# Kernel optimization log

Hardware: AMD Instinct MI355X
Metric: run time of the kernel (lower is better)

## Reference

```python
import jax, jax.numpy as jnp
import numpy as np

NUM_TYPES = 60
TOK_DIM = 128
DIM_TOK = TOK_DIM + 1          # +1 sentinel bucket
SMALL = 2
C = NUM_TYPES + DIM_TOK + SMALL  # 191 channels
STEPS = 10
BLOCKS = 5
NTYPES_E = 3
N = 4000
E = 12000
G = 32
LN_EPS = 1e-5


def setup_inputs() -> dict:
    key = jax.random.key(0)
    ks = jax.random.split(key, 12)
    p = lambda k, shape: jax.random.normal(k, shape, dtype=jnp.float32) * 0.02
    return dict(
        x_small=jax.random.uniform(ks[0], (N, SMALL), dtype=jnp.float32),
        conv_w=p(ks[1], (BLOCKS, NTYPES_E, STEPS, C, C)),
        gru_wih=p(ks[2], (BLOCKS, NTYPES_E, 3 * C, C)),
        gru_whh=p(ks[3], (BLOCKS, NTYPES_E, 3 * C, C)),
        gru_bih=jnp.zeros((BLOCKS, NTYPES_E, 3 * C), jnp.float32),
        gru_bhh=jnp.zeros((BLOCKS, NTYPES_E, 3 * C), jnp.float32),
        ln_w=jnp.ones((BLOCKS, C), jnp.float32),
        ln_b=jnp.zeros((BLOCKS, C), jnp.float32),
        head_w1=p(ks[4], (C, C)),
        head_b1=jnp.zeros((C,), jnp.float32),
        head_w2=p(ks[5], (C, 2)),
        head_b2=jnp.zeros((2,), jnp.float32),
        x_type=jax.random.randint(ks[6], (N,), 0, NUM_TYPES),
        x_tok=jax.random.randint(ks[7], (N,), 0, DIM_TOK),
        edge_index=jax.random.randint(ks[8], (2, E), 0, N),
        edge_type=jax.random.randint(ks[9], (E,), 0, NTYPES_E),
        batch=jnp.sort(jax.random.randint(ks[10], (N,), 0, G)),
    )


def reference(x_small, conv_w, gru_wih, gru_whh, gru_bih, gru_bhh,
              ln_w, ln_b, head_w1, head_b1, head_w2, head_b2,
              x_type, x_tok, edge_index, edge_type, batch):
    n = x_type.shape[0]
    # build_features: one-hot type || one-hot hashed token || small floats
    h_type = jax.nn.one_hot(x_type, NUM_TYPES, dtype=jnp.float32)
    h_tok = jax.nn.one_hot(jnp.clip(x_tok, 0, DIM_TOK - 1), DIM_TOK, dtype=jnp.float32)
    h = jnp.concatenate([h_type, h_tok, x_small], axis=1)  # [N, C]
    src, dst = edge_index[0], edge_index[1]

    def gated_conv(h0, w_steps, wih, whh, bih, bhh, emask):
        # PyG GatedGraphConv: per step, m = x @ W_i; scatter-add m[src]->dst; x = GRUCell(agg, x)
        def step(x, wi):
            m = x @ wi  # [N, C]
            agg = jax.ops.segment_sum(m[src] * emask[:, None], dst, num_segments=n)
            gi = agg @ wih.T + bih  # [N, 3C] input gates (r,z,n order as in torch)
            gh = x @ whh.T + bhh
            ir, iz, ic = jnp.split(gi, 3, axis=-1)
            hr, hz, hc = jnp.split(gh, 3, axis=-1)
            r = jax.nn.sigmoid(ir + hr)
            z = jax.nn.sigmoid(iz + hz)
            c = jnp.tanh(ic + r * hc)
            return (1.0 - z) * c + z * x, None
        x, _ = jax.lax.scan(step, h0, w_steps)
        return x

    for b in range(BLOCKS):
        h_msg = jnp.zeros_like(h)
        for t in range(NTYPES_E):
            # edge-type masking as zero-weight scatter (same math as boolean slicing)
            emask = (edge_type == t).astype(h.dtype)
            h_msg = h_msg + gated_conv(h, conv_w[b, t], gru_wih[b, t], gru_whh[b, t],
                                       gru_bih[b, t], gru_bhh[b, t], emask)
        x = h + h_msg
        mu = jnp.mean(x, axis=-1, keepdims=True)
        var = jnp.mean((x - mu) ** 2, axis=-1, keepdims=True)
        h = jax.nn.relu((x - mu) * jax.lax.rsqrt(var + LN_EPS) * ln_w[b] + ln_b[b])
        # dropout is identity in eval mode

    # global_mean_pool
    counts = jax.ops.segment_sum(jnp.ones((n,), h.dtype), batch, num_segments=G)
    hg = jax.ops.segment_sum(h, batch, num_segments=G) / jnp.maximum(counts, 1.0)[:, None]
    z1 = jax.nn.relu(hg @ head_w1 + head_b1)
    return z1 @ head_w2 + head_b2  # [G, 2] logits
```

## Files before the change

### kernel.cpp

```cpp
#include <hip/hip_runtime.h>
#include <math.h>

#define N_NODES 4000
#define CC 191
#define CP 192
#define NT 3
#define NB 5
#define NS 10
#define EE 12000
#define GG 32
#define THREE_C 573
#define NC (N_NODES * CP)
#define NPAD 576

typedef __attribute__((ext_vector_type(8))) short short8;
typedef __attribute__((ext_vector_type(4))) float f32x4;

__device__ __forceinline__ unsigned short f2bf(float f) {
    unsigned u = __float_as_uint(f);
    unsigned r = (u + 0x7fffu + ((u >> 16) & 1u)) >> 16;
    return (unsigned short)r;
}
__device__ __forceinline__ float bf2f(unsigned short s) {
    return __uint_as_float(((unsigned)s) << 16);
}
__device__ __forceinline__ float dot4(float4 a, float4 b) {
    return a.x * b.x + a.y * b.y + a.z * b.z + a.w * b.w;
}
__device__ __forceinline__ void dma16(const void* g, void* l) {
    __builtin_amdgcn_global_load_lds(
        (const __attribute__((address_space(1))) unsigned int*)g,
        (__attribute__((address_space(3))) unsigned int*)l, 16, 0, 0);
}

__global__ void k_build_h(const float* __restrict__ xs, const int* __restrict__ xtype,
                          const int* __restrict__ xtok, float* __restrict__ h) {
    int idx = blockIdx.x * 256 + threadIdx.x;
    if (idx >= NC) return;
    int i = idx / CP, c = idx % CP;
    float v = 0.f;
    if (c < 60) {
        v = (xtype[i] == c) ? 1.f : 0.f;
    } else if (c < 189) {
        int tk = xtok[i];
        tk = tk < 0 ? 0 : (tk > 128 ? 128 : tk);
        v = (tk == c - 60) ? 1.f : 0.f;
    } else if (c < CC) {
        v = xs[i * 2 + (c - 189)];
    }
    h[idx] = v;
}

__global__ void k_pad_conv(const float* __restrict__ w, float* __restrict__ wp) {
    long idx = (long)blockIdx.x * 256 + threadIdx.x;
    if (idx >= 150L * 192 * 192) return;
    int b = (int)(idx / (192 * 192));
    int r = (int)((idx / 192) % 192);
    int c = (int)(idx % 192);
    wp[idx] = (r < CC && c < CC) ? w[(long)b * CC * CC + (long)r * CC + c] : 0.f;
}

__global__ void k_pad573(const float* __restrict__ w, float* __restrict__ wp, int batches) {
    long tot = (long)batches * THREE_C * CP;
    long idx = (long)blockIdx.x * 256 + threadIdx.x;
    if (idx >= tot) return;
    int b = (int)(idx / (THREE_C * CP));
    int r = (int)((idx / CP) % THREE_C);
    int c = (int)(idx % CP);
    wp[idx] = (c < CC) ? w[((long)b * THREE_C + r) * CC + c] : 0.f;
}

__global__ void k_edge_count(const int* __restrict__ ei, const int* __restrict__ et,
                             int* __restrict__ cnt) {
    int e = blockIdx.x * 256 + threadIdx.x;
    if (e >= EE) return;
    atomicAdd(&cnt[et[e] * N_NODES + ei[EE + e]], 1);
}

__global__ void k_scan(const int* __restrict__ cnt, int* __restrict__ off, int* __restrict__ fill) {
    const int TOT = NT * N_NODES;
    const int CH = (TOT + 255) / 256;
    __shared__ int ls[256];
    int tid = threadIdx.x;
    int base = tid * CH;
    int s = 0;
    for (int u = 0; u < CH; u++) {
        int idx = base + u;
        if (idx < TOT) s += cnt[idx];
    }
    ls[tid] = s;
    __syncthreads();
    for (int d = 1; d < 256; d <<= 1) {
        int v = 0;
        if (tid >= d) v = ls[tid - d];
        __syncthreads();
        if (tid >= d) ls[tid] += v;
        __syncthreads();
    }
    int run = (tid > 0) ? ls[tid - 1] : 0;
    for (int u = 0; u < CH; u++) {
        int idx = base + u;
        if (idx < TOT) {
            off[idx] = run;
            fill[idx] = run;
            run += cnt[idx];
        }
    }
    if (tid == 255) off[TOT] = run;
}

__global__ void k_edge_fill(const int* __restrict__ ei, const int* __restrict__ et,
                            int* __restrict__ fill, int* __restrict__ csrc) {
    int e = blockIdx.x * 256 + threadIdx.x;
    if (e >= EE) return;
    int pos = atomicAdd(&fill[et[e] * N_NODES + ei[EE + e]], 1);
    csrc[pos] = ei[e];
}

__global__ __launch_bounds__(256) void k_fmat(const float* __restrict__ wih_p,
                                              const float* __restrict__ conv_wp,
                                              float* __restrict__ F_t, int b) {
    int ts = blockIdx.z;
    int t = ts / NS;
    int j30 = blockIdx.x * 32;
    int k0 = blockIdx.y * 64;
    const float* A = wih_p + (long)(b * 3 + t) * THREE_C * CP;
    const float* B = conv_wp + ((long)b * 30 + ts) * 192 * 192;
    __shared__ float sA[32 * 52];
    __shared__ float sB[64 * 52];
    int tid = threadIdx.x;
    int tj = tid % 32;
    int tn = tid / 32;
    float acc0[4] = {0, 0, 0, 0}, acc1[4] = {0, 0, 0, 0};
    for (int kb = 0; kb < 4; kb++) {
        int q0 = kb * 48;
        for (int idx = tid; idx < 32 * 12; idx += 256) {
            int row = idx / 12, c4 = idx % 12;
            int j3 = j30 + row; j3 = j3 < THREE_C ? j3 : THREE_C - 1;
            *(float4*)(sA + row * 52 + c4 * 4) = *(const float4*)(A + (long)j3 * CP + q0 + c4 * 4);
        }
        for (int idx = tid; idx < 64 * 12; idx += 256) {
            int row = idx / 12, c4 = idx % 12;
            *(float4*)(sB + row * 52 + c4 * 4) = *(const float4*)(B + (long)(k0 + row) * CP + q0 + c4 * 4);
        }
        __syncthreads();
        #pragma unroll 3
        for (int q4 = 0; q4 < 12; q4++) {
            float4 bv0 = *(const float4*)(sB + tj * 52 + q4 * 4);
            float4 bv1 = *(const float4*)(sB + (tj + 32) * 52 + q4 * 4);
            #pragma unroll
            for (int u = 0; u < 4; u++) {
                float4 av = *(const float4*)(sA + (tn + 8 * u) * 52 + q4 * 4);
                acc0[u] += dot4(av, bv0);
                acc1[u] += dot4(av, bv1);
            }
        }
        __syncthreads();
    }
    #pragma unroll
    for (int u = 0; u < 4; u++) {
        int j3 = j30 + tn + 8 * u;
        if (j3 < THREE_C) {
            F_t[((long)ts * THREE_C + j3) * CP + k0 + tj] = acc0[u];
            F_t[((long)ts * THREE_C + j3) * CP + k0 + tj + 32] = acc1[u];
        }
    }
}

__global__ void k_convF(const float* __restrict__ F_t, unsigned short* __restrict__ FH,
                        unsigned short* __restrict__ FL) {
    long idx = (long)blockIdx.x * 256 + threadIdx.x;
    if (idx >= 30L * NPAD * CP) return;
    int k = (int)(idx % CP);
    int p = (int)((idx / CP) % NPAD);
    int ts = (int)(idx / ((long)NPAD * CP));
    int B0 = p / 96, pr = p % 96;
    int v = pr >> 4, u = pr & 15;
    int g = v % 3;
    int j = B0 * 32 + (v / 3) * 16 + u;
    float val = 0.f;
    if (j < CC) val = F_t[((long)ts * THREE_C + g * CC + j) * CP + k];
    unsigned short hi = f2bf(val);
    FH[idx] = hi;
    FL[idx] = f2bf(val - bf2f(hi));
}

__global__ void k_convW(const float* __restrict__ whh_p, unsigned short* __restrict__ WH,
                        unsigned short* __restrict__ WL, int b) {
    long idx = (long)blockIdx.x * 256 + threadIdx.x;
    if (idx >= 3L * NPAD * CP) return;
    int k = (int)(idx % CP);
    int p = (int)((idx / CP) % NPAD);
    int t = (int)(idx / ((long)NPAD * CP));
    int B0 = p / 96, pr = p % 96;
    int v = pr >> 4, u = pr & 15;
    int g = v % 3;
    int j = B0 * 32 + (v / 3) * 16 + u;
    float val = 0.f;
    if (j < CC) val = whh_p[((long)(b * 3 + t) * THREE_C + g * CC + j) * CP + k];
    unsigned short hi = f2bf(val);
    WH[idx] = hi;
    WL[idx] = f2bf(val - bf2f(hi));
}

__global__ void k_split3(const float* __restrict__ h, unsigned short* __restrict__ XH,
                         unsigned short* __restrict__ XL) {
    int idx = blockIdx.x * 256 + threadIdx.x;
    if (idx >= NC) return;
    float f = h[idx];
    unsigned short hi = f2bf(f);
    unsigned short lo = f2bf(f - bf2f(hi));
    #pragma unroll
    for (int t = 0; t < NT; t++) {
        XH[(long)t * NC + idx] = hi;
        XL[(long)t * NC + idx] = lo;
    }
}

__global__ void k_agg(const unsigned short* __restrict__ XH, const unsigned short* __restrict__ XL,
                      unsigned short* __restrict__ AH, unsigned short* __restrict__ AL,
                      const int* __restrict__ off, const int* __restrict__ csrc) {
    int node = blockIdx.x;
    int t = blockIdx.y;
    int k = threadIdx.x;
    const unsigned short* Xh = XH + (long)t * NC;
    const unsigned short* Xl = XL + (long)t * NC;
    int e0 = off[t * N_NODES + node];
    int e1 = off[t * N_NODES + node + 1];
    float s = 0.f;
    for (int e = e0; e < e1; e++) {
        long base = (long)csrc[e] * CP + k;
        s += bf2f(Xh[base]) + bf2f(Xl[base]);
    }
    unsigned short hi = f2bf(s);
    long o = ((long)t * N_NODES + node) * CP + k;
    AH[o] = hi;
    AL[o] = f2bf(s - bf2f(hi));
}

__global__ __launch_bounds__(256, 2) void k_step(
        const unsigned short* __restrict__ XcH, const unsigned short* __restrict__ XcL,
        const unsigned short* __restrict__ AgH, const unsigned short* __restrict__ AgL,
        const unsigned short* __restrict__ FH, const unsigned short* __restrict__ FL,
        const unsigned short* __restrict__ WH, const unsigned short* __restrict__ WL,
        const float* __restrict__ bih, const float* __restrict__ bhh,
        unsigned short* __restrict__ XnH, unsigned short* __restrict__ XnL,
        int b, int s) {
    const int t = blockIdx.z;
    const int ts = t * NS + s;
    const int M0 = blockIdx.x * 128;
    const int N0 = blockIdx.y * 96;

    __shared__ __align__(16) char smem[57344];

    const int tid = threadIdx.x;
    const int lane = tid & 63;
    const int wave = tid >> 6;
    const int wm = wave & 1;
    const int wn = wave >> 1;
    const int l15 = lane & 15;
    const int kb = lane >> 4;
    const int quad = lane >> 4;

    const unsigned short* gA[4];
    gA[0] = XcH + (size_t)t * NC;
    gA[1] = AgH + (size_t)t * NC;
    gA[2] = XcL + (size_t)t * NC;
    gA[3] = AgL + (size_t)t * NC;
    const unsigned short* gB[4];
    gB[0] = FH + (size_t)ts * NPAD * CP;
    gB[1] = WH + (size_t)t * NPAD * CP;
    gB[2] = FL + (size_t)ts * NPAD * CP;
    gB[3] = WL + (size_t)t * NPAD * CP;

    f32x4 accGI[4][3], accGH[4][3];
    #pragma unroll
    for (int mi = 0; mi < 4; mi++)
        #pragma unroll
        for (int nj = 0; nj < 3; nj++) {
            accGI[mi][nj] = (f32x4){0.f, 0.f, 0.f, 0.f};
            accGH[mi][nj] = (f32x4){0.f, 0.f, 0.f, 0.f};
        }

    const int ldso = (tid & 192) << 4;
    const int qsA = tid & 3;
    const int rA_lo = tid >> 2;

    for (int k = 0; k < 6; k++) {
        const int ko = k * 32;
        __syncthreads();
        #pragma unroll
        for (int i = 0; i < 8; i++) {
            int a = i >> 1;
            int r = (i & 1) * 64 + rA_lo;
            int q = qsA ^ ((r >> 1) & 3);
            int node = M0 + r; node = node < N_NODES ? node : N_NODES - 1;
            dma16(gA[a] + (size_t)node * CP + ko + q * 8, smem + i * 4096 + ldso);
        }
        #pragma unroll
        for (int i = 0; i < 6; i++) {
            int c = i * 256 + tid;
            int a = c / 384;
            int rem = c - a * 384;
            int r = rem >> 2, qs = rem & 3;
            int q = qs ^ ((r >> 1) & 3);
            dma16(gB[a] + (size_t)(N0 + r) * CP + ko + q * 8, smem + 32768 + i * 4096 + ldso);
        }
        __syncthreads();

        short8 xh[4], gh[4], xl[4], gl[4];
        #pragma unroll
        for (int mi = 0; mi < 4; mi++) {
            int r = wm * 64 + mi * 16 + l15;
            int sl = (r * 4 + (kb ^ ((r >> 1) & 3))) * 16;
            xh[mi] = *(const short8*)(smem + sl);
            gh[mi] = *(const short8*)(smem + 8192 + sl);
            xl[mi] = *(const short8*)(smem + 16384 + sl);
            gl[mi] = *(const short8*)(smem + 24576 + sl);
        }
        short8 fh[3], wh[3], fl[3], wl[3];
        #pragma unroll
        for (int nj = 0; nj < 3; nj++) {
            int r = wn * 48 + nj * 16 + l15;
            int sl = (r * 4 + (kb ^ ((r >> 1) & 3))) * 16;
            fh[nj] = *(const short8*)(smem + 32768 + sl);
            wh[nj] = *(const short8*)(smem + 38912 + sl);
            fl[nj] = *(const short8*)(smem + 45056 + sl);
            wl[nj] = *(const short8*)(smem + 51200 + sl);
        }
        #pragma unroll
        for (int mi = 0; mi < 4; mi++)
            #pragma unroll
            for (int nj = 0; nj < 3; nj++) {
                accGI[mi][nj] = __builtin_amdgcn_mfma_f32_16x16x32_bf16(
                    gh[mi], fh[nj], accGI[mi][nj], 0, 0, 0);
                accGI[mi][nj] = __builtin_amdgcn_mfma_f32_16x16x32_bf16(
                    gl[mi], fh[nj], accGI[mi][nj], 0, 0, 0);
                accGI[mi][nj] = __builtin_amdgcn_mfma_f32_16x16x32_bf16(
                    gh[mi], fl[nj], accGI[mi][nj], 0, 0, 0);
                accGH[mi][nj] = __builtin_amdgcn_mfma_f32_16x16x32_bf16(
                    xh[mi], wh[nj], accGH[mi][nj], 0, 0, 0);
                accGH[mi][nj] = __builtin_amdgcn_mfma_f32_16x16x32_bf16(
                    xl[mi], wh[nj], accGH[mi][nj], 0, 0, 0);
                accGH[mi][nj] = __builtin_amdgcn_mfma_f32_16x16x32_bf16(
                    xh[mi], wl[nj], accGH[mi][nj], 0, 0, 0);
            }
    }

    const int J = blockIdx.y * 32 + wn * 16 + l15;
    const bool jv = (J < CC);
    const int Je = jv ? J : 0;
    const int bo = (b * 3 + t) * THREE_C;
    const float bir = bih[bo + Je], biz = bih[bo + CC + Je], bic = bih[bo + 2 * CC + Je];
    const float bhr = bhh[bo + Je], bhz = bhh[bo + CC + Je], bhc = bhh[bo + 2 * CC + Je];
    #pragma unroll
    for (int mi = 0; mi < 4; mi++) {
        #pragma unroll
        for (int r = 0; r < 4; r++) {
            int node = M0 + wm * 64 + mi * 16 + quad * 4 + r;
            if (node < N_NODES && jv) {
                size_t xi = (size_t)(t * N_NODES + node) * CP + J;
                float xold = bf2f(XcH[xi]) + bf2f(XcL[xi]);
                float rr = 1.f / (1.f + expf(-(accGI[mi][0][r] + bir + accGH[mi][0][r] + bhr)));
                float zz = 1.f / (1.f + expf(-(accGI[mi][1][r] + biz + accGH[mi][1][r] + bhz)));
                float cg = tanhf(accGI[mi][2][r] + bic + rr * (accGH[mi][2][r] + bhc));
                float outv = (1.f - zz) * cg + zz * xold;
                unsigned short oh = f2bf(outv);
                XnH[xi] = oh;
                XnL[xi] = f2bf(outv - bf2f(oh));
            }
        }
    }
}

__global__ void k_ln(float* __restrict__ h, const unsigned short* __restrict__ XH,
                     const unsigned short* __restrict__ XL,
                     const float* __restrict__ lnw, const float* __restrict__ lnb, int b) {
    int i = blockIdx.x;
    int c = threadIdx.x;
    long base = (long)i * CP + c;
    float v = 0.f;
    if (c < CC) {
        v = h[base];
        #pragma unroll
        for (int t = 0; t < NT; t++)
            v += bf2f(XH[(long)t * NC + base]) + bf2f(XL[(long)t * NC + base]);
    }
    float sv = v;
    for (int o = 32; o > 0; o >>= 1) sv += __shfl_down(sv, o);
    __shared__ float ls[3];
    __shared__ float bc[2];
    if ((threadIdx.x & 63) == 0) ls[threadIdx.x >> 6] = sv;
    __syncthreads();
    if (threadIdx.x == 0) bc[0] = (ls[0] + ls[1] + ls[2]) / (float)CC;
    __syncthreads();
    float mu = bc[0];
    float d = (c < CC) ? (v - mu) : 0.f;
    float s2 = d * d;
    for (int o = 32; o > 0; o >>= 1) s2 += __shfl_down(s2, o);
    __syncthreads();
    if ((threadIdx.x & 63) == 0) ls[threadIdx.x >> 6] = s2;
    __syncthreads();
    if (threadIdx.x == 0) bc[1] = (ls[0] + ls[1] + ls[2]) / (float)CC;
    __syncthreads();
    float var = bc[1];
    float y = 0.f;
    if (c < CC) {
        y = d * rsqrtf(var + 1e-5f) * lnw[b * CC + c] + lnb[b * CC + c];
        y = y > 0.f ? y : 0.f;
    }
    h[base] = y;
}

__global__ void k_pool(const float* __restrict__ h, const int* __restrict__ batch,
                       float* __restrict__ hg, float* __restrict__ gcnt) {
    int idx = blockIdx.x * 256 + threadIdx.x;
    if (idx >= NC) return;
    int i = idx / CP, c = idx % CP;
    int g = batch[i];
    if (c < CC) atomicAdd(&hg[g * CP + c], h[idx]);
    if (c == 0) atomicAdd(&gcnt[g], 1.f);
}

__global__ void k_head1(const float* __restrict__ hg, const float* __restrict__ gcnt,
                        const float* __restrict__ w1, const float* __restrict__ b1,
                        float* __restrict__ z1) {
    int g = blockIdx.x;
    int jcol = threadIdx.x;
    if (jcol >= CC) return;
    float inv = 1.f / fmaxf(gcnt[g], 1.f);
    float acc = 0.f;
    for (int k = 0; k < CC; k++) acc += hg[g * CP + k] * inv * w1[k * CC + jcol];
    acc += b1[jcol];
    z1[g * CP + jcol] = fmaxf(acc, 0.f);
}

__global__ void k_head2(const float* __restrict__ z1, const float* __restrict__ w2,
                        const float* __restrict__ b2, float* __restrict__ out) {
    int idx = threadIdx.x;
    if (idx >= GG * 2) return;
    int g = idx / 2, o = idx % 2;
    float acc = 0.f;
    for (int k = 0; k < CC; k++) acc += z1[g * CP + k] * w2[k * 2 + o];
    out[g * 2 + o] = acc + b2[o];
}

extern "C" void kernel_launch(void* const* d_in, const int* in_sizes, int n_in,
                              void* d_out, int out_size, void* d_ws, size_t ws_size,
                              hipStream_t stream) {
    const float* xs   = (const float*)d_in[0];
    const float* conv = (const float*)d_in[1];
    const float* wih  = (const float*)d_in[2];
    const float* whh  = (const float*)d_in[3];
    const float* bih  = (const float*)d_in[4];
    const float* bhh  = (const float*)d_in[5];
    const float* lnw  = (const float*)d_in[6];
    const float* lnb  = (const float*)d_in[7];
    const float* hw1  = (const float*)d_in[8];
    const float* hb1  = (const float*)d_in[9];
    const float* hw2  = (const float*)d_in[10];
    const float* hb2  = (const float*)d_in[11];
    const int* xtype  = (const int*)d_in[12];
    const int* xtok   = (const int*)d_in[13];
    const int* ei     = (const int*)d_in[14];
    const int* et     = (const int*)d_in[15];
    const int* batch  = (const int*)d_in[16];
    float* out = (float*)d_out;

    char* ws = (char*)d_ws;
    size_t o = 0;
    auto alloc = [&](size_t nbytes) {
        size_t r = o;
        o = (o + nbytes + 255) & ~(size_t)255;
        return r;
    };
    float* h      = (float*)(ws + alloc((size_t)NC * 4));
    float* F_t    = (float*)(ws + alloc((size_t)30 * THREE_C * CP * 4));
    float* wih_p  = (float*)(ws + alloc((size_t)15 * THREE_C * CP * 4));
    float* whh_p  = (float*)(ws + alloc((size_t)15 * THREE_C * CP * 4));
    float* convp  = (float*)(ws + alloc((size_t)150 * 192 * 192 * 4));
    unsigned short* FH  = (unsigned short*)(ws + alloc((size_t)30 * NPAD * CP * 2));
    unsigned short* FL  = (unsigned short*)(ws + alloc((size_t)30 * NPAD * CP * 2));
    unsigned short* WH  = (unsigned short*)(ws + alloc((size_t)3 * NPAD * CP * 2));
    unsigned short* WL  = (unsigned short*)(ws + alloc((size_t)3 * NPAD * CP * 2));
    unsigned short* XAh = (unsigned short*)(ws + alloc((size_t)NT * NC * 2));
    unsigned short* XAl = (unsigned short*)(ws + alloc((size_t)NT * NC * 2));
    unsigned short* XBh = (unsigned short*)(ws + alloc((size_t)NT * NC * 2));
    unsigned short* XBl = (unsigned short*)(ws + alloc((size_t)NT * NC * 2));
    unsigned short* AggH = (unsigned short*)(ws + alloc((size_t)NT * NC * 2));
    unsigned short* AggL = (unsigned short*)(ws + alloc((size_t)NT * NC * 2));
    float* hg     = (float*)(ws + alloc((size_t)GG * CP * 4));
    float* gcnt   = (float*)(ws + alloc((size_t)GG * 4));
    float* z1buf  = (float*)(ws + alloc((size_t)GG * CP * 4));
    int* cnt      = (int*)(ws + alloc((size_t)NT * N_NODES * 4));
    int* offb     = (int*)(ws + alloc((size_t)(NT * N_NODES + 1) * 4));
    int* fillb    = (int*)(ws + alloc((size_t)NT * N_NODES * 4));
    int* csrc     = (int*)(ws + alloc((size_t)EE * 4));
    (void)ws_size; (void)n_in; (void)in_sizes; (void)out_size;

    hipMemsetAsync(cnt, 0, (size_t)NT * N_NODES * 4, stream);
    hipMemsetAsync(hg, 0, (size_t)GG * CP * 4, stream);
    hipMemsetAsync(gcnt, 0, (size_t)GG * 4, stream);

    k_build_h<<<(NC + 255) / 256, 256, 0, stream>>>(xs, xtype, xtok, h);
    k_pad_conv<<<(int)((150L * 192 * 192 + 255) / 256), 256, 0, stream>>>(conv, convp);
    k_pad573<<<(int)(((long)15 * THREE_C * CP + 255) / 256), 256, 0, stream>>>(wih, wih_p, 15);
    k_pad573<<<(int)(((long)15 * THREE_C * CP + 255) / 256), 256, 0, stream>>>(whh, whh_p, 15);
    k_edge_count<<<(EE + 255) / 256, 256, 0, stream>>>(ei, et, cnt);
    k_scan<<<1, 256, 0, stream>>>(cnt, offb, fillb);
    k_edge_fill<<<(EE + 255) / 256, 256, 0, stream>>>(ei, et, fillb, csrc);

    for (int b = 0; b < NB; b++) {
        dim3 fg((THREE_C + 31) / 32, 3, 30);
        k_fmat<<<fg, 256, 0, stream>>>(wih_p, convp, F_t, b);
        k_convF<<<(int)((30L * NPAD * CP + 255) / 256), 256, 0, stream>>>(F_t, FH, FL);
        k_convW<<<(int)((3L * NPAD * CP + 255) / 256), 256, 0, stream>>>(whh_p, WH, WL, b);
        k_split3<<<(NC + 255) / 256, 256, 0, stream>>>(h, XAh, XAl);
        unsigned short *curH = XAh, *curL = XAl, *nxtH = XBh, *nxtL = XBl;
        for (int s = 0; s < NS; s++) {
            k_agg<<<dim3(N_NODES, NT), CP, 0, stream>>>(curH, curL, AggH, AggL, offb, csrc);
            dim3 sg(32, 6, NT);
            k_step<<<sg, 256, 0, stream>>>(curH, curL, AggH, AggL, FH, FL, WH, WL,
                                           bih, bhh, nxtH, nxtL, b, s);
            unsigned short* t1 = curH; curH = nxtH; nxtH = t1;
            unsigned short* t2 = curL; curL = nxtL; nxtL = t2;
        }
        k_ln<<<N_NODES, CP, 0, stream>>>(h, XAh, XAl, lnw, lnb, b);
    }

    k_pool<<<(NC + 255) / 256, 256, 0, stream>>>(h, batch, hg, gcnt);
    k_head1<<<GG, CP, 0, stream>>>(hg, gcnt, hw1, hb1, z1buf);
    k_head2<<<1, 64, 0, stream>>>(z1buf, hw2, hb2, out);
}
```

Baseline: 2.746 ms.

## Fuse edge aggregation into GRU step kernel and move weight-fusion GEMM to MFMA

Removes the separate per-step aggregation kernel. Each step block now gathers neighbour sums for its node tile straight into shared memory as split bf16 hi/lo operands, which avoids writing and re-reading the Agg buffers and saves 50 launches. The per-block F = W_ih·conv_w product now runs on bf16x3 MFMA with direct emission of the gate-permuted hi/lo layout, replacing the fp32 FMA GEMM and its conversion kernels. Weight padding and splitting are hoisted to a one-time setup pass. The trade-off is redundant gathers: the 6 N-tile blocks sharing a node tile each repeat the same aggregation, and the serial edge loop sits inside the k-loop.

```diff
diff --git a/kernel.cpp b/kernel.cpp
--- a/kernel.cpp
+++ b/kernel.cpp
@@ -23,9 +23,6 @@
 }
 __device__ __forceinline__ float bf2f(unsigned short s) {
     return __uint_as_float(((unsigned)s) << 16);
-}
-__device__ __forceinline__ float dot4(float4 a, float4 b) {
-    return a.x * b.x + a.y * b.y + a.z * b.z + a.w * b.w;
 }
 __device__ __forceinline__ void dma16(const void* g, void* l) {
     __builtin_amdgcn_global_load_lds(
@@ -51,23 +48,38 @@
     h[idx] = v;
 }
 
-__global__ void k_pad_conv(const float* __restrict__ w, float* __restrict__ wp) {
-    long idx = (long)blockIdx.x * 256 + threadIdx.x;
-    if (idx >= 150L * 192 * 192) return;
-    int b = (int)(idx / (192 * 192));
-    int r = (int)((idx / 192) % 192);
-    int c = (int)(idx % 192);
-    wp[idx] = (r < CC && c < CC) ? w[(long)b * CC * CC + (long)r * CC + c] : 0.f;
-}
-
-__global__ void k_pad573(const float* __restrict__ w, float* __restrict__ wp, int batches) {
-    long tot = (long)batches * THREE_C * CP;
+__global__ void k_split_gates(const float* __restrict__ src, unsigned short* __restrict__ H,
+                              unsigned short* __restrict__ L, int nbt) {
+    long tot = (long)nbt * NPAD * CP;
     long idx = (long)blockIdx.x * 256 + threadIdx.x;
     if (idx >= tot) return;
-    int b = (int)(idx / (THREE_C * CP));
-    int r = (int)((idx / CP) % THREE_C);
-    int c = (int)(idx % CP);
-    wp[idx] = (c < CC) ? w[((long)b * THREE_C + r) * CC + c] : 0.f;
+    int q = (int)(idx % CP);
+    int p = (int)((idx / CP) % NPAD);
+    int bt = (int)(idx / ((long)NPAD * CP));
+    int B0 = p / 96, pr = p % 96;
+    int v = pr >> 4, u = pr & 15;
+    int g = v % 3;
+    int j = B0 * 32 + (v / 3) * 16 + u;
+    float val = 0.f;
+    if (j < CC && q < CC) val = src[((long)bt * THREE_C + g * CC + j) * CC + q];
+    unsigned short hi = f2bf(val);
+    H[idx] = hi;
+    L[idx] = f2bf(val - bf2f(hi));
+}
+
+__global__ void k_split_conv(const float* __restrict__ src, unsigned short* __restrict__ H,
+                             unsigned short* __restrict__ L) {
+    long tot = 150L * 192 * 192;
+    long idx = (long)blockIdx.x * 256 + threadIdx.x;
+    if (idx >= tot) return;
+    int q = (int)(idx % 192);
+    int k = (int)((idx / 192) % 192);
+    int ts = (int)(idx / (192 * 192));
+    float val = 0.f;
+    if (k < CC && q < CC) val = src[((long)ts * CC + k) * CC + q];
+    unsigned short hi = f2bf(val);
+    H[idx] = hi;
+    L[idx] = f2bf(val - bf2f(hi));
 }
 
 __global__ void k_edge_count(const int* __restrict__ ei, const int* __restrict__ et,
@@ -117,90 +129,95 @@
     csrc[pos] = ei[e];
 }
 
-__global__ __launch_bounds__(256) void k_fmat(const float* __restrict__ wih_p,
-                                              const float* __restrict__ conv_wp,
-                                              float* __restrict__ F_t, int b) {
-    int ts = blockIdx.z;
-    int t = ts / NS;
-    int j30 = blockIdx.x * 32;
-    int k0 = blockIdx.y * 64;
-    const float* A = wih_p + (long)(b * 3 + t) * THREE_C * CP;
-    const float* B = conv_wp + ((long)b * 30 + ts) * 192 * 192;
-    __shared__ float sA[32 * 52];
-    __shared__ float sB[64 * 52];
-    int tid = threadIdx.x;
-    int tj = tid % 32;
-    int tn = tid / 32;
-    float acc0[4] = {0, 0, 0, 0}, acc1[4] = {0, 0, 0, 0};
-    for (int kb = 0; kb < 4; kb++) {
-        int q0 = kb * 48;
-        for (int idx = tid; idx < 32 * 12; idx += 256) {
-            int row = idx / 12, c4 = idx % 12;
-            int j3 = j30 + row; j3 = j3 < THREE_C ? j3 : THREE_C - 1;
-            *(float4*)(sA + row * 52 + c4 * 4) = *(const float4*)(A + (long)j3 * CP + q0 + c4 * 4);
-        }
-        for (int idx = tid; idx < 64 * 12; idx += 256) {
-            int row = idx / 12, c4 = idx % 12;
-            *(float4*)(sB + row * 52 + c4 * 4) = *(const float4*)(B + (long)(k0 + row) * CP + q0 + c4 * 4);
-        }
+__global__ __launch_bounds__(256, 4) void k_fmat_mfma(
+        const unsigned short* __restrict__ AH, const unsigned short* __restrict__ AL,
+        const unsigned short* __restrict__ BH, const unsigned short* __restrict__ BL,
+        unsigned short* __restrict__ FH, unsigned short* __restrict__ FL, int b) {
+    const int ts = blockIdx.z;
+    const int t = ts / NS;
+    const int M0 = blockIdx.x * 96;
+    const int N0 = blockIdx.y * 96;
+    __shared__ __align__(16) char smem[24576];
+
+    const int tid = threadIdx.x;
+    const int lane = tid & 63;
+    const int wave = tid >> 6;
+    const int wm = wave & 1;
+    const int wn = wave >> 1;
+    const int l15 = lane & 15;
+    const int kb = lane >> 4;
+    const int ldso = (tid & 192) << 4;
+
+    const unsigned short* gA[2];
+    gA[0] = AH + (size_t)(b * 3 + t) * NPAD * CP;
+    gA[1] = AL + (size_t)(b * 3 + t) * NPAD * CP;
+    const unsigned short* gB[2];
+    gB[0] = BH + (size_t)(b * 30 + ts) * 192 * 192;
+    gB[1] = BL + (size_t)(b * 30 + ts) * 192 * 192;
+
+    f32x4 acc[3][3];
+    #pragma unroll
+    for (int mi = 0; mi < 3; mi++)
+        #pragma unroll
+        for (int nj = 0; nj < 3; nj++) acc[mi][nj] = (f32x4){0.f, 0.f, 0.f, 0.f};
+
+    for (int k = 0; k < 6; k++) {
+        const int ko = k * 32;
         __syncthreads();
-        #pragma unroll 3
-        for (int q4 = 0; q4 < 12; q4++) {
-            float4 bv0 = *(const float4*)(sB + tj * 52 + q4 * 4);
-            float4 bv1 = *(const float4*)(sB + (tj + 32) * 52 + q4 * 4);
+        #pragma unroll
+        for (int i = 0; i < 6; i++) {
+            int c = i * 256 + tid;
+            int a = c / 384;
+            int rem = c - a * 384;
+            int r = rem >> 2, qs = rem & 3;
+            int q = qs ^ ((r >> 1) & 3);
+            const unsigned short* g = (a < 2) ? gA[a] : gB[a - 2];
+            int row = ((a < 2) ? M0 : N0) + r;
+            dma16(g + (size_t)row * CP + ko + q * 8, smem + (i * 256 & ~255) * 16 + ldso);
+        }
+        __syncthreads();
+
+        short8 ah[3], al[3], bh[3], bl[3];
+        #pragma unroll
+        for (int mi = 0; mi < 3; mi++) {
+            int r = wm * 48 + mi * 16 + l15;
+            int sl = (r * 4 + (kb ^ ((r >> 1) & 3))) * 16;
+            ah[mi] = *(const short8*)(smem + sl);
+            al[mi] = *(const short8*)(smem + 6144 + sl);
+        }
+        #pragma unroll
+        for (int nj = 0; nj < 3; nj++) {
+            int r = wn * 48 + nj * 16 + l15;
+            int sl = (r * 4 + (kb ^ ((r >> 1) & 3))) * 16;
+            bh[nj] = *(const short8*)(smem + 12288 + sl);
+            bl[nj] = *(const short8*)(smem + 18432 + sl);
+        }
+        #pragma unroll
+        for (int mi = 0; mi < 3; mi++)
             #pragma unroll
-            for (int u = 0; u < 4; u++) {
-                float4 av = *(const float4*)(sA + (tn + 8 * u) * 52 + q4 * 4);
-                acc0[u] += dot4(av, bv0);
-                acc1[u] += dot4(av, bv1);
+            for (int nj = 0; nj < 3; nj++) {
+                acc[mi][nj] = __builtin_amdgcn_mfma_f32_16x16x32_bf16(
+                    ah[mi], bh[nj], acc[mi][nj], 0, 0, 0);
+                acc[mi][nj] = __builtin_amdgcn_mfma_f32_16x16x32_bf16(
+                    al[mi], bh[nj], acc[mi][nj], 0, 0, 0);
+                acc[mi][nj] = __builtin_amdgcn_mfma_f32_16x16x32_bf16(
+                    ah[mi], bl[nj], acc[mi][nj], 0, 0, 0);
             }
-        }
-        __syncthreads();
     }
     #pragma unroll
-    for (int u = 0; u < 4; u++) {
-        int j3 = j30 + tn + 8 * u;
-        if (j3 < THREE_C) {
-            F_t[((long)ts * THREE_C + j3) * CP + k0 + tj] = acc0[u];
-            F_t[((long)ts * THREE_C + j3) * CP + k0 + tj + 32] = acc1[u];
-        }
-    }
-}
-
-__global__ void k_convF(const float* __restrict__ F_t, unsigned short* __restrict__ FH,
-                        unsigned short* __restrict__ FL) {
-    long idx = (long)blockIdx.x * 256 + threadIdx.x;
-    if (idx >= 30L * NPAD * CP) return;
-    int k = (int)(idx % CP);
-    int p = (int)((idx / CP) % NPAD);
-    int ts = (int)(idx / ((long)NPAD * CP));
-    int B0 = p / 96, pr = p % 96;
-    int v = pr >> 4, u = pr & 15;
-    int g = v % 3;
-    int j = B0 * 32 + (v / 3) * 16 + u;
-    float val = 0.f;
-    if (j < CC) val = F_t[((long)ts * THREE_C + g * CC + j) * CP + k];
-    unsigned short hi = f2bf(val);
-    FH[idx] = hi;
-    FL[idx] = f2bf(val - bf2f(hi));
-}
-
-__global__ void k_convW(const float* __restrict__ whh_p, unsigned short* __restrict__ WH,
-                        unsigned short* __restrict__ WL, int b) {
-    long idx = (long)blockIdx.x * 256 + threadIdx.x;
-    if (idx >= 3L * NPAD * CP) return;
-    int k = (int)(idx % CP);
-    int p = (int)((idx / CP) % NPAD);
-    int t = (int)(idx / ((long)NPAD * CP));
-    int B0 = p / 96, pr = p % 96;
-    int v = pr >> 4, u = pr & 15;
-    int g = v % 3;
-    int j = B0 * 32 + (v / 3) * 16 + u;
-    float val = 0.f;
-    if (j < CC) val = whh_p[((long)(b * 3 + t) * THREE_C + g * CC + j) * CP + k];
-    unsigned short hi = f2bf(val);
-    WH[idx] = hi;
-    WL[idx] = f2bf(val - bf2f(hi));
+    for (int mi = 0; mi < 3; mi++)
+        #pragma unroll
+        for (int nj = 0; nj < 3; nj++)
+            #pragma unroll
+            for (int r = 0; r < 4; r++) {
+                int p = M0 + wm * 48 + mi * 16 + kb * 4 + r;
+                int kc = N0 + wn * 48 + nj * 16 + l15;
+                float val = acc[mi][nj][r];
+                unsigned short hi = f2bf(val);
+                size_t o = ((size_t)ts * NPAD + p) * CP + kc;
+                FH[o] = hi;
+                FL[o] = f2bf(val - bf2f(hi));
+            }
 }
 
 __global__ void k_split3(const float* __restrict__ h, unsigned short* __restrict__ XH,
@@ -217,33 +234,12 @@
     }
 }
 
-__global__ void k_agg(const unsigned short* __restrict__ XH, const unsigned short* __restrict__ XL,
-                      unsigned short* __restrict__ AH, unsigned short* __restrict__ AL,
-                      const int* __restrict__ off, const int* __restrict__ csrc) {
-    int node = blockIdx.x;
-    int t = blockIdx.y;
-    int k = threadIdx.x;
-    const unsigned short* Xh = XH + (long)t * NC;
-    const unsigned short* Xl = XL + (long)t * NC;
-    int e0 = off[t * N_NODES + node];
-    int e1 = off[t * N_NODES + node + 1];
-    float s = 0.f;
-    for (int e = e0; e < e1; e++) {
-        long base = (long)csrc[e] * CP + k;
-        s += bf2f(Xh[base]) + bf2f(Xl[base]);
-    }
-    unsigned short hi = f2bf(s);
-    long o = ((long)t * N_NODES + node) * CP + k;
-    AH[o] = hi;
-    AL[o] = f2bf(s - bf2f(hi));
-}
-
 __global__ __launch_bounds__(256, 2) void k_step(
         const unsigned short* __restrict__ XcH, const unsigned short* __restrict__ XcL,
-        const unsigned short* __restrict__ AgH, const unsigned short* __restrict__ AgL,
         const unsigned short* __restrict__ FH, const unsigned short* __restrict__ FL,
         const unsigned short* __restrict__ WH, const unsigned short* __restrict__ WL,
         const float* __restrict__ bih, const float* __restrict__ bhh,
+        const int* __restrict__ off, const int* __restrict__ csrc,
         unsigned short* __restrict__ XnH, unsigned short* __restrict__ XnL,
         int b, int s) {
     const int t = blockIdx.z;
@@ -260,18 +256,23 @@
     const int wn = wave >> 1;
     const int l15 = lane & 15;
     const int kb = lane >> 4;
-    const int quad = lane >> 4;
-
-    const unsigned short* gA[4];
-    gA[0] = XcH + (size_t)t * NC;
-    gA[1] = AgH + (size_t)t * NC;
-    gA[2] = XcL + (size_t)t * NC;
-    gA[3] = AgL + (size_t)t * NC;
+
+    const unsigned short* Xh = XcH + (size_t)t * NC;
+    const unsigned short* Xl = XcL + (size_t)t * NC;
     const unsigned short* gB[4];
     gB[0] = FH + (size_t)ts * NPAD * CP;
-    gB[1] = WH + (size_t)t * NPAD * CP;
+    gB[1] = WH + (size_t)(b * 3 + t) * NPAD * CP;
     gB[2] = FL + (size_t)ts * NPAD * CP;
-    gB[3] = WL + (size_t)t * NPAD * CP;
+    gB[3] = WL + (size_t)(b * 3 + t) * NPAD * CP;
+
+    const int gr = tid >> 1;
+    const int ghalf = tid & 1;
+    const int gnode = M0 + gr;
+    int ge0 = 0, ge1 = 0;
+    if (gnode < N_NODES) {
+        ge0 = off[t * N_NODES + gnode];
+        ge1 = off[t * N_NODES + gnode + 1];
+    }
 
     f32x4 accGI[4][3], accGH[4][3];
     #pragma unroll
@@ -290,12 +291,12 @@
         const int ko = k * 32;
         __syncthreads();
         #pragma unroll
-        for (int i = 0; i < 8; i++) {
+        for (int i = 0; i < 4; i++) {
             int a = i >> 1;
             int r = (i & 1) * 64 + rA_lo;
             int q = qsA ^ ((r >> 1) & 3);
             int node = M0 + r; node = node < N_NODES ? node : N_NODES - 1;
-            dma16(gA[a] + (size_t)node * CP + ko + q * 8, smem + i * 4096 + ldso);
+            dma16((a ? Xl : Xh) + (size_t)node * CP + ko + q * 8, smem + i * 4096 + ldso);
         }
         #pragma unroll
         for (int i = 0; i < 6; i++) {
@@ -306,6 +307,42 @@
             int q = qs ^ ((r >> 1) & 3);
             dma16(gB[a] + (size_t)(N0 + r) * CP + ko + q * 8, smem + 32768 + i * 4096 + ldso);
         }
+        {
+            float sacc[16];
+            #pragma unroll
+            for (int u = 0; u < 16; u++) sacc[u] = 0.f;
+            const int chb = ko + ghalf * 16;
+            for (int e = ge0; e < ge1; e++) {
+                int srcn = csrc[e];
+                const unsigned short* ph = Xh + (size_t)srcn * CP + chb;
+                const unsigned short* pl = Xl + (size_t)srcn * CP + chb;
+                short8 vh0 = *(const short8*)ph;
+                short8 vh1 = *(const short8*)(ph + 8);
+                short8 vl0 = *(const short8*)pl;
+                short8 vl1 = *(const short8*)(pl + 8);
+                #pragma unroll
+                for (int u = 0; u < 8; u++) {
+                    sacc[u]     += bf2f((unsigned short)vh0[u]) + bf2f((unsigned short)vl0[u]);
+                    sacc[8 + u] += bf2f((unsigned short)vh1[u]) + bf2f((unsigned short)vl1[u]);
+                }
+            }
+            #pragma unroll
+            for (int qi = 0; qi < 2; qi++) {
+                short8 vh, vl;
+                #pragma unroll
+                for (int u = 0; u < 8; u++) {
+                    float v = sacc[qi * 8 + u];
+                    unsigned short hi = f2bf(v);
+                    vh[u] = (short)hi;
+                    vl[u] = (short)f2bf(v - bf2f(hi));
+                }
+                int q = ghalf * 2 + qi;
+                int qphys = q ^ ((gr >> 1) & 3);
+                int addr = (gr * 4 + qphys) * 16;
+                *(short8*)(smem + 16384 + addr) = vh;
+                *(short8*)(smem + 24576 + addr) = vl;
+            }
+        }
         __syncthreads();
 
         short8 xh[4], gh[4], xl[4], gl[4];
@@ -314,8 +351,8 @@
             int r = wm * 64 + mi * 16 + l15;
             int sl = (r * 4 + (kb ^ ((r >> 1) & 3))) * 16;
             xh[mi] = *(const short8*)(smem + sl);
-            gh[mi] = *(const short8*)(smem + 8192 + sl);
-            xl[mi] = *(const short8*)(smem + 16384 + sl);
+            xl[mi] = *(const short8*)(smem + 8192 + sl);
+            gh[mi] = *(const short8*)(smem + 16384 + sl);
             gl[mi] = *(const short8*)(smem + 24576 + sl);
         }
         short8 fh[3], wh[3], fl[3], wl[3];
@@ -357,7 +394,7 @@
     for (int mi = 0; mi < 4; mi++) {
         #pragma unroll
         for (int r = 0; r < 4; r++) {
-            int node = M0 + wm * 64 + mi * 16 + quad * 4 + r;
+            int node = M0 + wm * 64 + mi * 16 + kb * 4 + r;
             if (node < N_NODES && jv) {
                 size_t xi = (size_t)(t * N_NODES + node) * CP + J;
                 float xold = bf2f(XcH[xi]) + bf2f(XcL[xi]);
@@ -475,20 +512,18 @@
         return r;
     };
     float* h      = (float*)(ws + alloc((size_t)NC * 4));
-    float* F_t    = (float*)(ws + alloc((size_t)30 * THREE_C * CP * 4));
-    float* wih_p  = (float*)(ws + alloc((size_t)15 * THREE_C * CP * 4));
-    float* whh_p  = (float*)(ws + alloc((size_t)15 * THREE_C * CP * 4));
-    float* convp  = (float*)(ws + alloc((size_t)150 * 192 * 192 * 4));
-    unsigned short* FH  = (unsigned short*)(ws + alloc((size_t)30 * NPAD * CP * 2));
-    unsigned short* FL  = (unsigned short*)(ws + alloc((size_t)30 * NPAD * CP * 2));
-    unsigned short* WH  = (unsigned short*)(ws + alloc((size_t)3 * NPAD * CP * 2));
-    unsigned short* WL  = (unsigned short*)(ws + alloc((size_t)3 * NPAD * CP * 2));
+    unsigned short* FH    = (unsigned short*)(ws + alloc((size_t)30 * NPAD * CP * 2));
+    unsigned short* FL    = (unsigned short*)(ws + alloc((size_t)30 * NPAD * CP * 2));
+    unsigned short* WHH   = (unsigned short*)(ws + alloc((size_t)15 * NPAD * CP * 2));
+    unsigned short* WHL   = (unsigned short*)(ws + alloc((size_t)15 * NPAD * CP * 2));
+    unsigned short* wihH  = (unsigned short*)(ws + alloc((size_t)15 * NPAD * CP * 2));
+    unsigned short* wihL  = (unsigned short*)(ws + alloc((size_t)15 * NPAD * CP * 2));
+    unsigned short* convH = (unsigned short*)(ws + alloc((size_t)150 * 192 * 192 * 2));
+    unsigned short* convL = (unsigned short*)(ws + alloc((size_t)150 * 192 * 192 * 2));
     unsigned short* XAh = (unsigned short*)(ws + alloc((size_t)NT * NC * 2));
     unsigned short* XAl = (unsigned short*)(ws + alloc((size_t)NT * NC * 2));
     unsigned short* XBh = (unsigned short*)(ws + alloc((size_t)NT * NC * 2));
     unsigned short* XBl = (unsigned short*)(ws + alloc((size_t)NT * NC * 2));
-    unsigned short* AggH = (unsigned short*)(ws + alloc((size_t)NT * NC * 2));
-    unsigned short* AggL = (unsigned short*)(ws + alloc((size_t)NT * NC * 2));
     float* hg     = (float*)(ws + alloc((size_t)GG * CP * 4));
     float* gcnt   = (float*)(ws + alloc((size_t)GG * 4));
     float* z1buf  = (float*)(ws + alloc((size_t)GG * CP * 4));
@@ -503,25 +538,21 @@
     hipMemsetAsync(gcnt, 0, (size_t)GG * 4, stream);
 
     k_build_h<<<(NC + 255) / 256, 256, 0, stream>>>(xs, xtype, xtok, h);
-    k_pad_conv<<<(int)((150L * 192 * 192 + 255) / 256), 256, 0, stream>>>(conv, convp);
-    k_pad573<<<(int)(((long)15 * THREE_C * CP + 255) / 256), 256, 0, stream>>>(wih, wih_p, 15);
-    k_pad573<<<(int)(((long)15 * THREE_C * CP + 255) / 256), 256, 0, stream>>>(whh, whh_p, 15);
+    k_split_gates<<<(int)((15L * NPAD * CP + 255) / 256), 256, 0, stream>>>(wih, wihH, wihL, 15);
+    k_split_gates<<<(int)((15L * NPAD * CP + 255) / 256), 256, 0, stream>>>(whh, WHH, WHL, 15);
+    k_split_conv<<<(int)((150L * 192 * 192 + 255) / 256), 256, 0, stream>>>(conv, convH, convL);
     k_edge_count<<<(EE + 255) / 256, 256, 0, stream>>>(ei, et, cnt);
     k_scan<<<1, 256, 0, stream>>>(cnt, offb, fillb);
     k_edge_fill<<<(EE + 255) / 256, 256, 0, stream>>>(ei, et, fillb, csrc);
 
     for (int b = 0; b < NB; b++) {
-        dim3 fg((THREE_C + 31) / 32, 3, 30);
-        k_fmat<<<fg, 256, 0, stream>>>(wih_p, convp, F_t, b);
-        k_convF<<<(int)((30L * NPAD * CP + 255) / 256), 256, 0, stream>>>(F_t, FH, FL);
-        k_convW<<<(int)((3L * NPAD * CP + 255) / 256), 256, 0, stream>>>(whh_p, WH, WL, b);
+        k_fmat_mfma<<<dim3(6, 2, 30), 256, 0, stream>>>(wihH, wihL, convH, convL, FH, FL, b);
         k_split3<<<(NC + 255) / 256, 256, 0, stream>>>(h, XAh, XAl);
         unsigned short *curH = XAh, *curL = XAl, *nxtH = XBh, *nxtL = XBl;
         for (int s = 0; s < NS; s++) {
-            k_agg<<<dim3(N_NODES, NT), CP, 0, stream>>>(curH, curL, AggH, AggL, offb, csrc);
             dim3 sg(32, 6, NT);
-            k_step<<<sg, 256, 0, stream>>>(curH, curL, AggH, AggL, FH, FL, WH, WL,
-                                           bih, bhh, nxtH, nxtL, b, s);
+            k_step<<<sg, 256, 0, stream>>>(curH, curL, FH, FL, WHH, WHL,
+                                           bih, bhh, offb, csrc, nxtH, nxtL, b, s);
             unsigned short* t1 = curH; curH = nxtH; nxtH = t1;
             unsigned short* t2 = curL; curL = nxtL; nxtL = t2;
         }
```

Measured after the change: 3.416 ms. 24.4% more time.
